# Kernel optimization log

Hardware: AMD Instinct MI355X
Metric: run time of the kernel (lower is better)

The kernel has to match this reference:

```python
import jax, jax.numpy as jnp
import numpy as np

NUM_HEADS = 16


def setup_inputs() -> dict:
    key = jax.random.key(0)
    k1, k2, k3, k4 = jax.random.split(key, 4)
    B, N, C = 4, 2048, 1024
    x = jax.random.normal(k1, (B, N, C), dtype=jnp.float32)
    g_info = jax.random.normal(k2, (2, 4, C), dtype=jnp.float32)
    qkv_w = jax.random.normal(k3, (3 * C, C), dtype=jnp.float32) * 0.02
    proj_w = jax.random.normal(k4, (C, C), dtype=jnp.float32) * 0.02
    proj_b = jnp.zeros((C,), dtype=jnp.float32)
    return {"x": x, "g_info": g_info, "qkv_w": qkv_w, "proj_w": proj_w, "proj_b": proj_b}


def reference(x, g_info, qkv_w, proj_w, proj_b):
    B, N, C = x.shape
    H = NUM_HEADS
    D = C // H
    scale = D ** -0.5
    # qkv projection (no bias): [B,N,3C] -> [B,N,3,H,D]
    qkv = (x @ qkv_w.T).reshape(B, N, 3, H, D)
    q, k, v = qkv[:, :, 0], qkv[:, :, 1], qkv[:, :, 2]  # each [B,N,H,D]
    # global-info fusion: g_info[0] -> (4,H,D); rows = q_g, k_g, v_g, t_g
    gl = g_info[0].reshape(4, H, D)
    q_g = gl[0][None, None]  # [1,1,H,D]
    k_g = gl[1][None, None]
    # NOTE: source computes min/max rescaled q_g/k_g but they are dead code;
    # the attention actually uses the unscaled additive fusion below.
    q_fused = q + q_g
    k_fused = k + k_g
    # memory_efficient_attention(q,k,v): softmax(q k^T / sqrt(D)) v
    attn = jnp.einsum("bqhd,bkhd->bhqk", q_fused, k_fused) * scale
    attn = jax.nn.softmax(attn, axis=-1)
    out = jnp.einsum("bhqk,bkhd->bqhd", attn, v).reshape(B, N, C)
    out = out @ proj_w.T + proj_b
    return (out, g_info[1:])
```

## Files before the change

kernel.cpp:

```cpp
#include <hip/hip_runtime.h>

typedef _Float16 h4 __attribute__((ext_vector_type(4)));
typedef _Float16 h8 __attribute__((ext_vector_type(8)));
typedef __fp16 fp16x2 __attribute__((ext_vector_type(2)));
typedef float f4 __attribute__((ext_vector_type(4)));
typedef float f16v __attribute__((ext_vector_type(16)));

#define MFMA16(a,b,c) __builtin_amdgcn_mfma_f32_16x16x32_f16(a, b, c, 0, 0, 0)
#define MFMA32(a,b,c) __builtin_amdgcn_mfma_f32_32x32x16_f16(a, b, c, 0, 0, 0)
#define EXP2(x) __builtin_amdgcn_exp2f(x)

__device__ __forceinline__ void gload_lds16(const _Float16* g, _Float16* l) {
    __builtin_amdgcn_global_load_lds((const __attribute__((address_space(1))) void*)g,
                                     (__attribute__((address_space(3))) void*)l, 16, 0, 0);
}

__device__ __forceinline__ void half_swap(float v, float& a, float& b) {
    unsigned x = __float_as_uint(v), y = x;
    asm("v_permlane32_swap_b32 %0, %1" : "+v"(x), "+v"(y));
    a = __uint_as_float(x); b = __uint_as_float(y);
}

__device__ __forceinline__ h8 ldfrag_sw(const _Float16* S, int R, int kk, int kq) {
    int b = kk * 4 + kq;
    return *(const h8*)(S + R * 64 + ((b ^ (R & 7)) * 8));
}

__device__ __forceinline__ void gemm_main(const _Float16* __restrict__ A, const _Float16* __restrict__ B,
                                          int K, int tM, int tN, int tid,
                                          _Float16* As, _Float16* Bs, f4 acc[4][4]) {
    int lane = tid & 63, w = tid >> 6;
    int wm = w >> 1, wn = w & 1;
    int ln = lane & 15, kq = lane >> 4;
    int r = tid >> 3;
    int sb = tid & 7;

    for (int k0 = 0; k0 < K; k0 += 64) {
#pragma unroll
        for (int it = 0; it < 4; ++it) {
            int row = r + it * 32;
            int srcb = sb ^ (row & 7);
            const _Float16* ga = A + (size_t)(tM * 128 + row) * K + k0 + srcb * 8;
            const _Float16* gb = B + (size_t)(tN * 128 + row) * K + k0 + srcb * 8;
            _Float16* la = As + ((tid & ~63) + it * 256) * 8;
            _Float16* lb = Bs + ((tid & ~63) + it * 256) * 8;
            gload_lds16(ga, la);
            gload_lds16(gb, lb);
        }
        __syncthreads();
#pragma unroll
        for (int kk = 0; kk < 2; ++kk) {
            h8 af[4], bf[4];
#pragma unroll
            for (int mi = 0; mi < 4; ++mi) af[mi] = ldfrag_sw(As, wm * 64 + mi * 16 + ln, kk, kq);
#pragma unroll
            for (int ni = 0; ni < 4; ++ni) bf[ni] = ldfrag_sw(Bs, wn * 64 + ni * 16 + ln, kk, kq);
#pragma unroll
            for (int mi = 0; mi < 4; ++mi)
#pragma unroll
                for (int ni = 0; ni < 4; ++ni) acc[mi][ni] = MFMA16(af[mi], bf[ni], acc[mi][ni]);
        }
        __syncthreads();
    }
}

__global__ __launch_bounds__(256) void k_cvt3(const float* __restrict__ x, const float* __restrict__ wq,
                                              const float* __restrict__ wp, _Float16* __restrict__ xh,
                                              _Float16* __restrict__ wqh, _Float16* __restrict__ wph) {
    const int NX = 1048576, NQ = 393216, NP = 131072;
    int stride = gridDim.x * blockDim.x;
    for (int s = blockIdx.x * blockDim.x + threadIdx.x; s < NX + NQ + NP; s += stride) {
        const float* src;
        _Float16* dst;
        int off;
        if (s < NX) { src = x; dst = xh; off = s; }
        else if (s < NX + NQ) { src = wq; dst = wqh; off = s - NX; }
        else { src = wp; dst = wph; off = s - NX - NQ; }
        float4 a = ((const float4*)src)[off * 2];
        float4 b = ((const float4*)src)[off * 2 + 1];
        h8 r = {(_Float16)a.x, (_Float16)a.y, (_Float16)a.z, (_Float16)a.w,
                (_Float16)b.x, (_Float16)b.y, (_Float16)b.z, (_Float16)b.w};
        ((h8*)dst)[off] = r;
    }
}

__global__ __launch_bounds__(256) void k_qkv(const _Float16* __restrict__ A, const _Float16* __restrict__ B,
                                             const float* __restrict__ g, _Float16* __restrict__ Qf,
                                             _Float16* __restrict__ Kf, _Float16* __restrict__ Vt) {
    __shared__ __align__(16) _Float16 As[128 * 64];
    __shared__ __align__(16) _Float16 Bs[128 * 64];
    int tid = threadIdx.x;
    int tN = blockIdx.x, tM = blockIdx.y;
    int lane = tid & 63, w = tid >> 6;
    int wm = w >> 1, wn = w & 1;
    int ln = lane & 15, kq = lane >> 4;

    f4 acc[4][4] = {};
    gemm_main(A, B, 1024, tM, tN, tid, As, Bs, acc);

#pragma unroll
    for (int mi = 0; mi < 4; ++mi) {
#pragma unroll
        for (int ni = 0; ni < 4; ++ni) {
#pragma unroll
            for (int r = 0; r < 4; ++r) {
                int gr = tM * 128 + wm * 64 + mi * 16 + kq * 4 + r;
                int gc = tN * 128 + wn * 64 + ni * 16 + ln;
                float val = acc[mi][ni][r];
                int which = gc >> 10;
                int c = gc & 1023, h = c >> 6, d = c & 63;
                int b = gr >> 11, n = gr & 2047;
                int bh = b * 16 + h;
                if (which == 0) {
                    val = (val + g[c]) * 0.18033688f;
                    Qf[((size_t)bh * 2048 + n) * 64 + d] = (_Float16)val;
                } else if (which == 1) {
                    val += g[1024 + c];
                    Kf[((size_t)bh * 2048 + n) * 64 + d] = (_Float16)val;
                } else {
                    Vt[((size_t)bh * 64 + d) * 2048 + n] = (_Float16)val;
                }
            }
        }
    }
}

__global__ __launch_bounds__(256) void k_attn(const _Float16* __restrict__ Qf, const _Float16* __restrict__ Kf,
                                              const _Float16* __restrict__ Vt, _Float16* __restrict__ Oa) {
    __shared__ __align__(16) _Float16 KV[2][2][64 * 64];
    int tid = threadIdx.x;
    int qt = blockIdx.x, bh = blockIdx.y;
    int lane = tid & 63, w = tid >> 6;
    int l31 = lane & 31, hi = lane >> 5;
    const _Float16* Qb = Qf + (size_t)bh * 2048 * 64;
    const _Float16* Kb = Kf + (size_t)bh * 2048 * 64;
    const _Float16* Vb = Vt + (size_t)bh * 64 * 2048;
    int qrow0 = qt * 128 + w * 32;

    int srow = tid >> 3, sblk = tid & 7;
    int sblk0 = (sblk ^ (srow & 7)) * 8;

#define STAGE(bufi, kvc)                                                                     \
    {                                                                                        \
        _Float16* lk = &KV[bufi][0][0] + ((tid & ~63)) * 8;                                  \
        _Float16* lv = &KV[bufi][1][0] + ((tid & ~63)) * 8;                                  \
        gload_lds16(Kb + (size_t)((kvc) + srow) * 64 + sblk0, lk);                           \
        gload_lds16(Kb + (size_t)((kvc) + srow + 32) * 64 + sblk0, lk + 2048);               \
        gload_lds16(Vb + (size_t)srow * 2048 + (kvc) + sblk0, lv);                           \
        gload_lds16(Vb + (size_t)(srow + 32) * 2048 + (kvc) + sblk0, lv + 2048);             \
    }

    h8 qfr[4];
#pragma unroll
    for (int dc = 0; dc < 4; ++dc)
        qfr[dc] = *(const h8*)(Qb + (size_t)(qrow0 + l31) * 64 + dc * 16 + hi * 8);

    f16v o0 = {}, o1 = {};
    float l_run = 0.f;

    STAGE(0, 0);
    __syncthreads();

    int cur = 0;
    for (int kvc = 0; kvc < 2048; kvc += 64) {
        if (kvc + 64 < 2048) STAGE(cur ^ 1, kvc + 64);

        const _Float16* Klc = &KV[cur][0][0];
        const _Float16* Vlc = &KV[cur][1][0];
        int sw = l31 & 7;

        f16v s0, s1;
#pragma unroll
        for (int r = 0; r < 16; ++r) { s0[r] = -4.f; s1[r] = -4.f; }
        __builtin_amdgcn_s_setprio(1);
#pragma unroll
        for (int dc = 0; dc < 4; ++dc) {
            int cb = dc * 2 + hi;
            h8 kf0 = *(const h8*)&Klc[l31 * 64 + ((cb ^ sw) * 8)];
            h8 kf1 = *(const h8*)&Klc[(32 + l31) * 64 + ((cb ^ sw) * 8)];
            s0 = MFMA32(kf0, qfr[dc], s0);
            s1 = MFMA32(kf1, qfr[dc], s1);
        }
        __builtin_amdgcn_s_setprio(0);

        float ps0[16], ps1[16];
#pragma unroll
        for (int r = 0; r < 16; ++r) ps0[r] = EXP2(s0[r]);
#pragma unroll
        for (int r = 0; r < 16; ++r) ps1[r] = EXP2(s1[r]);

        float t[16];
#pragma unroll
        for (int i = 0; i < 16; ++i) t[i] = ps0[i] + ps1[i];
#pragma unroll
        for (int i = 0; i < 8; ++i) t[i] += t[i + 8];
#pragma unroll
        for (int i = 0; i < 4; ++i) t[i] += t[i + 4];
        l_run += (t[0] + t[1]) + (t[2] + t[3]);

        unsigned W[16];
#pragma unroll
        for (int i = 0; i < 8; ++i) {
            union { fp16x2 h; unsigned u; } a, b;
            a.h = __builtin_amdgcn_cvt_pkrtz(ps0[2 * i], ps0[2 * i + 1]);
            b.h = __builtin_amdgcn_cvt_pkrtz(ps1[2 * i], ps1[2 * i + 1]);
            W[i] = a.u;
            W[8 + i] = b.u;
        }

        __builtin_amdgcn_s_setprio(1);
#pragma unroll
        for (int t2 = 0; t2 < 2; ++t2) {
#pragma unroll
            for (int kcl = 0; kcl < 2; ++kcl) {
                unsigned w0 = W[t2 * 8 + kcl * 4 + 0], w1 = W[t2 * 8 + kcl * 4 + 1];
                unsigned w2 = W[t2 * 8 + kcl * 4 + 2], w3 = W[t2 * 8 + kcl * 4 + 3];
                asm("v_permlane32_swap_b32 %0, %1" : "+v"(w0), "+v"(w2));
                asm("v_permlane32_swap_b32 %0, %1" : "+v"(w1), "+v"(w3));
                union { unsigned u[4]; h8 v; } pf;
                pf.u[0] = w0; pf.u[1] = w1; pf.u[2] = w2; pf.u[3] = w3;
                int cb = (t2 * 2 + kcl) * 2 + hi;
                h8 vf0 = *(const h8*)&Vlc[l31 * 64 + ((cb ^ sw) * 8)];
                h8 vf1 = *(const h8*)&Vlc[(32 + l31) * 64 + ((cb ^ sw) * 8)];
                o0 = MFMA32(pf.v, vf0, o0);
                o1 = MFMA32(pf.v, vf1, o1);
            }
        }
        __builtin_amdgcn_s_setprio(0);

        __syncthreads();
        cur ^= 1;
    }
#undef STAGE

    float la, lb;
    half_swap(l_run, la, lb);
    float inv = 1.f / (la + lb);
    int b = bh >> 4, h = bh & 15;
#pragma unroll
    for (int r = 0; r < 16; ++r) {
        int qloc = (r & 3) + 8 * (r >> 2) + 4 * hi;
        float iv = __shfl(inv, qloc, 64);
        size_t base = ((size_t)b * 2048 + qrow0 + qloc) * 1024 + h * 64;
        Oa[base + l31] = (_Float16)(o0[r] * iv);
        Oa[base + 32 + l31] = (_Float16)(o1[r] * iv);
    }
}

__global__ __launch_bounds__(256) void k_proj(const _Float16* __restrict__ A, const _Float16* __restrict__ B,
                                              const float* __restrict__ bias, float* __restrict__ out) {
    __shared__ __align__(16) _Float16 As[128 * 64];
    __shared__ __align__(16) _Float16 Bs[128 * 64];
    int tid = threadIdx.x;
    int tN = blockIdx.x, tM = blockIdx.y;
    int lane = tid & 63, w = tid >> 6;
    int wm = w >> 1, wn = w & 1;
    int ln = lane & 15, kq = lane >> 4;

    f4 acc[4][4] = {};
    gemm_main(A, B, 1024, tM, tN, tid, As, Bs, acc);

#pragma unroll
    for (int mi = 0; mi < 4; ++mi) {
#pragma unroll
        for (int ni = 0; ni < 4; ++ni) {
#pragma unroll
            for (int r = 0; r < 4; ++r) {
                int gr = tM * 128 + wm * 64 + mi * 16 + kq * 4 + r;
                int gc = tN * 128 + wn * 64 + ni * 16 + ln;
                out[(size_t)gr * 1024 + gc] = acc[mi][ni][r] + bias[gc];
            }
        }
    }
}

__global__ __launch_bounds__(256) void k_tail(const float* __restrict__ g, float* __restrict__ out) {
    int i = blockIdx.x * 256 + threadIdx.x;
    out[i] = g[4096 + i];
}

extern "C" void kernel_launch(void* const* d_in, const int* in_sizes, int n_in,
                              void* d_out, int out_size, void* d_ws, size_t ws_size,
                              hipStream_t stream) {
    const float* x = (const float*)d_in[0];
    const float* g = (const float*)d_in[1];
    const float* wq = (const float*)d_in[2];
    const float* wp = (const float*)d_in[3];
    const float* pb = (const float*)d_in[4];
    float* out = (float*)d_out;

    _Float16* xh = (_Float16*)d_ws;
    _Float16* wqh = xh + 8388608;
    _Float16* wph = wqh + 3145728;
    _Float16* Qf = wph + 1048576;
    _Float16* Kf = Qf + 8388608;
    _Float16* Vt = Kf + 8388608;
    _Float16* Oa = xh;

    k_cvt3<<<2048, 256, 0, stream>>>(x, wq, wp, xh, wqh, wph);
    k_qkv<<<dim3(24, 64), 256, 0, stream>>>(xh, wqh, g, Qf, Kf, Vt);
    k_attn<<<dim3(16, 64), 256, 0, stream>>>(Qf, Kf, Vt, Oa);
    k_proj<<<dim3(8, 64), 256, 0, stream>>>(Oa, wph, pb, out);
    k_tail<<<16, 256, 0, stream>>>(g, out + 8388608);
}
```

Before: 237.0 us.

## Double-buffer LDS tiles in GEMM main loop to overlap loads with MFMA

Result: faster. 230.9 us (-2.5%).

```diff
diff --git a/kernel.cpp b/kernel.cpp
--- a/kernel.cpp
+++ b/kernel.cpp
@@ -35,33 +35,46 @@
     int r = tid >> 3;
     int sb = tid & 7;
 
+#define GSTAGE(buf, k0)                                                                     \
+    {                                                                                       \
+        _Pragma("unroll")                                                                   \
+        for (int it = 0; it < 4; ++it) {                                                    \
+            int row = r + it * 32;                                                          \
+            int srcb = sb ^ (row & 7);                                                      \
+            gload_lds16(A + (size_t)(tM * 128 + row) * K + (k0) + srcb * 8,                 \
+                        As + (buf) * 8192 + ((tid & ~63) + it * 256) * 8);                  \
+            gload_lds16(B + (size_t)(tN * 128 + row) * K + (k0) + srcb * 8,                 \
+                        Bs + (buf) * 8192 + ((tid & ~63) + it * 256) * 8);                  \
+        }                                                                                   \
+    }
+
+    GSTAGE(0, 0);
+    __syncthreads();
+
+    int cur = 0;
     for (int k0 = 0; k0 < K; k0 += 64) {
-#pragma unroll
-        for (int it = 0; it < 4; ++it) {
-            int row = r + it * 32;
-            int srcb = sb ^ (row & 7);
-            const _Float16* ga = A + (size_t)(tM * 128 + row) * K + k0 + srcb * 8;
-            const _Float16* gb = B + (size_t)(tN * 128 + row) * K + k0 + srcb * 8;
-            _Float16* la = As + ((tid & ~63) + it * 256) * 8;
-            _Float16* lb = Bs + ((tid & ~63) + it * 256) * 8;
-            gload_lds16(ga, la);
-            gload_lds16(gb, lb);
-        }
-        __syncthreads();
+        if (k0 + 64 < K) GSTAGE(cur ^ 1, k0 + 64);
+
+        const _Float16* Asc = As + cur * 8192;
+        const _Float16* Bsc = Bs + cur * 8192;
+        __builtin_amdgcn_s_setprio(1);
 #pragma unroll
         for (int kk = 0; kk < 2; ++kk) {
             h8 af[4], bf[4];
 #pragma unroll
-            for (int mi = 0; mi < 4; ++mi) af[mi] = ldfrag_sw(As, wm * 64 + mi * 16 + ln, kk, kq);
-#pragma unroll
-            for (int ni = 0; ni < 4; ++ni) bf[ni] = ldfrag_sw(Bs, wn * 64 + ni * 16 + ln, kk, kq);
+            for (int mi = 0; mi < 4; ++mi) af[mi] = ldfrag_sw(Asc, wm * 64 + mi * 16 + ln, kk, kq);
+#pragma unroll
+            for (int ni = 0; ni < 4; ++ni) bf[ni] = ldfrag_sw(Bsc, wn * 64 + ni * 16 + ln, kk, kq);
 #pragma unroll
             for (int mi = 0; mi < 4; ++mi)
 #pragma unroll
                 for (int ni = 0; ni < 4; ++ni) acc[mi][ni] = MFMA16(af[mi], bf[ni], acc[mi][ni]);
         }
+        __builtin_amdgcn_s_setprio(0);
         __syncthreads();
-    }
+        cur ^= 1;
+    }
+#undef GSTAGE
 }
 
 __global__ __launch_bounds__(256) void k_cvt3(const float* __restrict__ x, const float* __restrict__ wq,
@@ -87,8 +100,8 @@
 __global__ __launch_bounds__(256) void k_qkv(const _Float16* __restrict__ A, const _Float16* __restrict__ B,
                                              const float* __restrict__ g, _Float16* __restrict__ Qf,
                                              _Float16* __restrict__ Kf, _Float16* __restrict__ Vt) {
-    __shared__ __align__(16) _Float16 As[128 * 64];
-    __shared__ __align__(16) _Float16 Bs[128 * 64];
+    __shared__ __align__(16) _Float16 As[2 * 128 * 64];
+    __shared__ __align__(16) _Float16 Bs[2 * 128 * 64];
     int tid = threadIdx.x;
     int tN = blockIdx.x, tM = blockIdx.y;
     int lane = tid & 63, w = tid >> 6;
@@ -249,8 +262,8 @@
 
 __global__ __launch_bounds__(256) void k_proj(const _Float16* __restrict__ A, const _Float16* __restrict__ B,
                                               const float* __restrict__ bias, float* __restrict__ out) {
-    __shared__ __align__(16) _Float16 As[128 * 64];
-    __shared__ __align__(16) _Float16 Bs[128 * 64];
+    __shared__ __align__(16) _Float16 As[2 * 128 * 64];
+    __shared__ __align__(16) _Float16 Bs[2 * 128 * 64];
     int tid = threadIdx.x;
     int tN = blockIdx.x, tM = blockIdx.y;
     int lane = tid & 63, w = tid >> 6;
```

## Use 256x256 double-buffered GEMM tiles with 8 waves for QKV and proj

Applied to the files above, without the earlier changes.

Result: slower. 248.7 us (+5.0%).

```diff
diff --git a/kernel.cpp b/kernel.cpp
--- a/kernel.cpp
+++ b/kernel.cpp
@@ -21,47 +21,98 @@
     a = __uint_as_float(x); b = __uint_as_float(y);
 }
 
-__device__ __forceinline__ h8 ldfrag_sw(const _Float16* S, int R, int kk, int kq) {
-    int b = kk * 4 + kq;
-    return *(const h8*)(S + R * 64 + ((b ^ (R & 7)) * 8));
-}
-
-__device__ __forceinline__ void gemm_main(const _Float16* __restrict__ A, const _Float16* __restrict__ B,
-                                          int K, int tM, int tN, int tid,
-                                          _Float16* As, _Float16* Bs, f4 acc[4][4]) {
-    int lane = tid & 63, w = tid >> 6;
-    int wm = w >> 1, wn = w & 1;
+__device__ __forceinline__ void gemm256(const _Float16* __restrict__ A, const _Float16* __restrict__ B,
+                                        int K, int tM, int tN, int tid,
+                                        _Float16* Al, _Float16* Bl, f4 acc[8][4]) {
+    int lane = tid & 63;
+    int wid = tid >> 6;
+    int wm2 = wid >> 2, wn4 = wid & 3;
     int ln = lane & 15, kq = lane >> 4;
-    int r = tid >> 3;
-    int sb = tid & 7;
-
-    for (int k0 = 0; k0 < K; k0 += 64) {
-#pragma unroll
-        for (int it = 0; it < 4; ++it) {
-            int row = r + it * 32;
-            int srcb = sb ^ (row & 7);
-            const _Float16* ga = A + (size_t)(tM * 128 + row) * K + k0 + srcb * 8;
-            const _Float16* gb = B + (size_t)(tN * 128 + row) * K + k0 + srcb * 8;
-            _Float16* la = As + ((tid & ~63) + it * 256) * 8;
-            _Float16* lb = Bs + ((tid & ~63) + it * 256) * 8;
-            gload_lds16(ga, la);
-            gload_lds16(gb, lb);
-        }
-        __syncthreads();
-#pragma unroll
-        for (int kk = 0; kk < 2; ++kk) {
-            h8 af[4], bf[4];
-#pragma unroll
-            for (int mi = 0; mi < 4; ++mi) af[mi] = ldfrag_sw(As, wm * 64 + mi * 16 + ln, kk, kq);
-#pragma unroll
-            for (int ni = 0; ni < 4; ++ni) bf[ni] = ldfrag_sw(Bs, wn * 64 + ni * 16 + ln, kk, kq);
-#pragma unroll
-            for (int mi = 0; mi < 4; ++mi)
-#pragma unroll
-                for (int ni = 0; ni < 4; ++ni) acc[mi][ni] = MFMA16(af[mi], bf[ni], acc[mi][ni]);
-        }
-        __syncthreads();
-    }
+    int NT = K >> 6;
+
+    h8 afr[4][2], bfr[2][2];
+
+#define STG(P, Lbase, buf, k0, tbase)                                                       \
+    { _Pragma("unroll")                                                                     \
+      for (int it = 0; it < 4; ++it) {                                                      \
+        int s = tid + it * 512;                                                             \
+        int row = s >> 3, blk = s & 7;                                                      \
+        gload_lds16(P + (size_t)((tbase) + row) * K + (k0) + ((blk ^ (row & 7)) * 8),       \
+                    Lbase + (buf) * 16384 + ((tid & ~63) + it * 512) * 8);                  \
+      } }
+
+#define LDA(qm, buf)                                                                        \
+    { _Pragma("unroll")                                                                     \
+      for (int mi = 0; mi < 4; ++mi) {                                                      \
+        int R = wm2 * 128 + ((qm) * 4 + mi) * 16 + ln;                                      \
+        _Pragma("unroll")                                                                   \
+        for (int kk = 0; kk < 2; ++kk) {                                                    \
+          int b = kk * 4 + kq;                                                              \
+          afr[mi][kk] = *(const h8*)(Al + (buf) * 16384 + R * 64 + ((b ^ (R & 7)) * 8));    \
+        } } }
+
+#define LDB(qn, buf)                                                                        \
+    { _Pragma("unroll")                                                                     \
+      for (int ni = 0; ni < 2; ++ni) {                                                      \
+        int R = wn4 * 64 + ((qn) * 2 + ni) * 16 + ln;                                       \
+        _Pragma("unroll")                                                                   \
+        for (int kk = 0; kk < 2; ++kk) {                                                    \
+          int b = kk * 4 + kq;                                                              \
+          bfr[ni][kk] = *(const h8*)(Bl + (buf) * 16384 + R * 64 + ((b ^ (R & 7)) * 8));    \
+        } } }
+
+#define MMA(qm, qn)                                                                         \
+    { _Pragma("unroll")                                                                     \
+      for (int mi = 0; mi < 4; ++mi)                                                        \
+        _Pragma("unroll")                                                                   \
+        for (int ni = 0; ni < 2; ++ni)                                                      \
+          _Pragma("unroll")                                                                 \
+          for (int kk = 0; kk < 2; ++kk)                                                    \
+            acc[(qm) * 4 + mi][(qn) * 2 + ni] =                                             \
+                MFMA16(afr[mi][kk], bfr[ni][kk], acc[(qm) * 4 + mi][(qn) * 2 + ni]); }
+
+#define WAITL  asm volatile("s_waitcnt lgkmcnt(0)" ::: "memory"); __builtin_amdgcn_sched_barrier(0);
+#define BARR   __builtin_amdgcn_s_barrier();
+#define SP1    __builtin_amdgcn_s_setprio(1);
+#define SP0    __builtin_amdgcn_s_setprio(0);
+
+    STG(A, Al, 0, 0, tM * 256);
+    STG(B, Bl, 0, 0, tN * 256);
+    asm volatile("s_waitcnt vmcnt(0)" ::: "memory");
+    BARR;
+
+    for (int t = 0; t < NT; ++t) {
+        int buf = t & 1, nb = buf ^ 1;
+        int kn = (t + 1) << 6;
+        bool pf = (t + 1) < NT;
+        LDA(0, buf); LDB(0, buf);
+        if (pf) STG(A, Al, nb, kn, tM * 256);
+        BARR; WAITL;
+        SP1; MMA(0, 0); SP0;
+        BARR;
+        LDB(1, buf);
+        if (pf) STG(B, Bl, nb, kn, tN * 256);
+        BARR; WAITL;
+        SP1; MMA(0, 1); SP0;
+        BARR;
+        LDA(1, buf);
+        BARR; WAITL;
+        SP1; MMA(1, 1); SP0;
+        BARR;
+        LDB(0, buf);
+        BARR; WAITL;
+        SP1; MMA(1, 0); SP0;
+        asm volatile("s_waitcnt vmcnt(0)" ::: "memory");
+        BARR;
+    }
+#undef STG
+#undef LDA
+#undef LDB
+#undef MMA
+#undef WAITL
+#undef BARR
+#undef SP1
+#undef SP0
 }
 
 __global__ __launch_bounds__(256) void k_cvt3(const float* __restrict__ x, const float* __restrict__ wq,
@@ -84,28 +135,28 @@
     }
 }
 
-__global__ __launch_bounds__(256) void k_qkv(const _Float16* __restrict__ A, const _Float16* __restrict__ B,
+__global__ __launch_bounds__(512) void k_qkv(const _Float16* __restrict__ A, const _Float16* __restrict__ B,
                                              const float* __restrict__ g, _Float16* __restrict__ Qf,
                                              _Float16* __restrict__ Kf, _Float16* __restrict__ Vt) {
-    __shared__ __align__(16) _Float16 As[128 * 64];
-    __shared__ __align__(16) _Float16 Bs[128 * 64];
+    __shared__ __align__(16) _Float16 Al[2 * 256 * 64];
+    __shared__ __align__(16) _Float16 Bl[2 * 256 * 64];
     int tid = threadIdx.x;
     int tN = blockIdx.x, tM = blockIdx.y;
-    int lane = tid & 63, w = tid >> 6;
-    int wm = w >> 1, wn = w & 1;
+    int lane = tid & 63, wid = tid >> 6;
+    int wm2 = wid >> 2, wn4 = wid & 3;
     int ln = lane & 15, kq = lane >> 4;
 
-    f4 acc[4][4] = {};
-    gemm_main(A, B, 1024, tM, tN, tid, As, Bs, acc);
-
-#pragma unroll
-    for (int mi = 0; mi < 4; ++mi) {
+    f4 acc[8][4] = {};
+    gemm256(A, B, 1024, tM, tN, tid, Al, Bl, acc);
+
+#pragma unroll
+    for (int mi = 0; mi < 8; ++mi) {
 #pragma unroll
         for (int ni = 0; ni < 4; ++ni) {
 #pragma unroll
             for (int r = 0; r < 4; ++r) {
-                int gr = tM * 128 + wm * 64 + mi * 16 + kq * 4 + r;
-                int gc = tN * 128 + wn * 64 + ni * 16 + ln;
+                int gr = tM * 256 + wm2 * 128 + mi * 16 + kq * 4 + r;
+                int gc = tN * 256 + wn4 * 64 + ni * 16 + ln;
                 float val = acc[mi][ni][r];
                 int which = gc >> 10;
                 int c = gc & 1023, h = c >> 6, d = c & 63;
@@ -247,27 +298,27 @@
     }
 }
 
-__global__ __launch_bounds__(256) void k_proj(const _Float16* __restrict__ A, const _Float16* __restrict__ B,
+__global__ __launch_bounds__(512) void k_proj(const _Float16* __restrict__ A, const _Float16* __restrict__ B,
                                               const float* __restrict__ bias, float* __restrict__ out) {
-    __shared__ __align__(16) _Float16 As[128 * 64];
-    __shared__ __align__(16) _Float16 Bs[128 * 64];
+    __shared__ __align__(16) _Float16 Al[2 * 256 * 64];
+    __shared__ __align__(16) _Float16 Bl[2 * 256 * 64];
     int tid = threadIdx.x;
     int tN = blockIdx.x, tM = blockIdx.y;
-    int lane = tid & 63, w = tid >> 6;
-    int wm = w >> 1, wn = w & 1;
+    int lane = tid & 63, wid = tid >> 6;
+    int wm2 = wid >> 2, wn4 = wid & 3;
     int ln = lane & 15, kq = lane >> 4;
 
-    f4 acc[4][4] = {};
-    gemm_main(A, B, 1024, tM, tN, tid, As, Bs, acc);
-
-#pragma unroll
-    for (int mi = 0; mi < 4; ++mi) {
+    f4 acc[8][4] = {};
+    gemm256(A, B, 1024, tM, tN, tid, Al, Bl, acc);
+
+#pragma unroll
+    for (int mi = 0; mi < 8; ++mi) {
 #pragma unroll
         for (int ni = 0; ni < 4; ++ni) {
 #pragma unroll
             for (int r = 0; r < 4; ++r) {
-                int gr = tM * 128 + wm * 64 + mi * 16 + kq * 4 + r;
-                int gc = tN * 128 + wn * 64 + ni * 16 + ln;
+                int gr = tM * 256 + wm2 * 128 + mi * 16 + kq * 4 + r;
+                int gc = tN * 256 + wn4 * 64 + ni * 16 + ln;
                 out[(size_t)gr * 1024 + gc] = acc[mi][ni][r] + bias[gc];
             }
         }
@@ -298,8 +349,8 @@
     _Float16* Oa = xh;
 
     k_cvt3<<<2048, 256, 0, stream>>>(x, wq, wp, xh, wqh, wph);
-    k_qkv<<<dim3(24, 64), 256, 0, stream>>>(xh, wqh, g, Qf, Kf, Vt);
+    k_qkv<<<dim3(12, 32), 512, 0, stream>>>(xh, wqh, g, Qf, Kf, Vt);
     k_attn<<<dim3(16, 64), 256, 0, stream>>>(Qf, Kf, Vt, Oa);
-    k_proj<<<dim3(8, 64), 256, 0, stream>>>(Oa, wph, pb, out);
+    k_proj<<<dim3(4, 32), 512, 0, stream>>>(Oa, wph, pb, out);
     k_tail<<<16, 256, 0, stream>>>(g, out + 8388608);
 }
```
